# Kernel tuning notes

Hardware: AMD Instinct MI355X
Metric: run time of the kernel (lower is better)

The kernel has to match this reference:

```python
import jax, jax.numpy as jnp
import numpy as np

N = 500000
P = 50000
IN_DIM = 9
H = 128
EPS = 1e-5


def _xavier(key, fan_in, fan_out, gain=0.5):
    std = gain * np.sqrt(2.0 / (fan_in + fan_out))
    return jax.random.normal(key, (fan_in, fan_out), dtype=jnp.float32) * std


def setup_inputs() -> dict:
    key = jax.random.key(0)
    kx, kid, k0, k1, k2 = jax.random.split(key, 5)
    x = jax.random.normal(kx, (N, IN_DIM), dtype=jnp.float32)
    # guarantee every polyline id in [0, P) appears so torch.unique inverse == ids
    ids = jnp.concatenate([jnp.arange(P, dtype=jnp.int64),
                           jax.random.randint(kid, (N - P,), 0, P, dtype=jnp.int64)])
    polyline_ids = jax.random.permutation(kid, ids)
    inp = {"x": x, "polyline_ids": polyline_ids,
           "W0": _xavier(k0, IN_DIM, H), "b0": jnp.zeros((H,), jnp.float32),
           "g0": jnp.ones((H,), jnp.float32), "be0": jnp.zeros((H,), jnp.float32),
           "W1": _xavier(k1, 2 * H, H), "b1": jnp.zeros((H,), jnp.float32),
           "g1": jnp.ones((H,), jnp.float32), "be1": jnp.zeros((H,), jnp.float32),
           "W2": _xavier(k2, 2 * H, H), "b2": jnp.zeros((H,), jnp.float32),
           "g2": jnp.ones((H,), jnp.float32), "be2": jnp.zeros((H,), jnp.float32)}
    return inp


def _encoder(h, W, b, g, be):
    # Linear -> LayerNorm -> ReLU (Dropout is identity in eval)
    z = h @ W + b
    mu = jnp.mean(z, axis=-1, keepdims=True)
    var = jnp.var(z, axis=-1, keepdims=True)
    z = (z - mu) * jax.lax.rsqrt(var + EPS) * g + be
    return jax.nn.relu(z)


def _seg_max(h, ids):
    m = jax.ops.segment_max(h, ids, num_segments=P)
    # torch scatter_reduce(amax, include_self=False) leaves empty rows at 0
    return jnp.where(jnp.isfinite(m), m, 0.0)


def reference(x, polyline_ids, W0, b0, g0, be0, W1, b1, g1, be1, W2, b2, g2, be2):
    ids = polyline_ids.astype(jnp.int32)  # all of [0,P) present -> inverse == ids
    h = _encoder(x, W0, b0, g0, be0)  # [N, H]
    for (W, b, g, be) in ((W1, b1, g1, be1), (W2, b2, g2, be2)):
        agg = _seg_max(h, ids)[ids]               # [N, H] broadcast of per-polyline max
        h = _encoder(jnp.concatenate([h, agg], axis=-1), W, b, g, be)
    polyline_features = _seg_max(h, ids)          # [P, H]
    unique_polylines = jnp.arange(P, dtype=polyline_ids.dtype)
    return polyline_features, unique_polylines
```

## Files before the change

kernel.cpp:

```cpp
#include <hip/hip_runtime.h>
#include <hip/hip_bf16.h>
#include <hip/hip_fp16.h>

#define N_PTS 500000
#define P_POLY 50000
#define IN_DIM 9
#define HDIM 128
#define EPSV 1e-5f
#define NG 7813
#define CAPR 96
#define SLOTS 32
#define HS 136
#define XS 40

typedef __attribute__((ext_vector_type(8))) short short8;
typedef __attribute__((ext_vector_type(4))) float floatx4;

__device__ __forceinline__ unsigned short f2h(float f) {
  return __half_as_ushort(__float2half(f));
}
__device__ __forceinline__ float h2f(unsigned short u) {
  return __half2float(__ushort_as_half(u));
}
__device__ __forceinline__ unsigned int pkmax(unsigned int a, unsigned int b) {
  unsigned int r;
  asm("v_pk_max_f16 %0, %1, %2" : "=v"(r) : "v"(a), "v"(b));
  return r;
}

__global__ __launch_bounds__(256) void k_count(
    const int* __restrict__ ids, unsigned int* __restrict__ cnt)
{
  int i = blockIdx.x * blockDim.x + threadIdx.x;
  if (i < N_PTS) atomicAdd(&cnt[ids[i]], 1u);
}

__global__ __launch_bounds__(256) void k_scanwp(
    const unsigned int* __restrict__ cnt, unsigned int* __restrict__ btot,
    const float* __restrict__ W0, const float* __restrict__ W1,
    const float* __restrict__ W2,
    unsigned short* __restrict__ Wt0,
    unsigned short* __restrict__ Wt1, unsigned short* __restrict__ Wb1,
    unsigned short* __restrict__ Wt2, unsigned short* __restrict__ Wb2)
{
  if (blockIdx.x < 196) {
    __shared__ unsigned int s[256];
    int t = threadIdx.x;
    int i = blockIdx.x * 256 + t;
    s[t] = (i < P_POLY) ? cnt[i] : 0u;
    __syncthreads();
    for (int d = 128; d > 0; d >>= 1) {
      if (t < d) s[t] += s[t + d];
      __syncthreads();
    }
    if (t == 0) btot[blockIdx.x] = s[0];
  } else if (blockIdx.x < 324) {
    int bw = blockIdx.x - 196;
#pragma unroll
    for (int t = 0; t < 2; ++t) {
      int idx = (bw * 2 + t) * 256 + threadIdx.x;
      int sel = idx >> 14;
      int e = idx & 16383;
      int c = e & 127;
      int k = e >> 7;
      const float* W = (sel < 2) ? W1 : W2;
      unsigned short* O = sel == 0 ? Wt1 : sel == 1 ? Wb1 : sel == 2 ? Wt2 : Wb2;
      int kg = k + ((sel & 1) ? 128 : 0);
      O[c * 128 + k] = f2h(W[kg * 128 + c]);
    }
  } else {
#pragma unroll
    for (int t = 0; t < 16; ++t) {
      int idx = t * 256 + threadIdx.x;
      int c = idx & 127;
      int k = idx >> 7;
      Wt0[c * 32 + k] = (k < IN_DIM) ? f2h(W0[k * 128 + c]) : (unsigned short)0;
    }
  }
}

__global__ __launch_bounds__(256) void k_scan2(
    const unsigned int* __restrict__ cnt, const unsigned int* __restrict__ btot,
    unsigned int* __restrict__ offsets, unsigned int* __restrict__ woff)
{
  __shared__ unsigned int s[256];
  __shared__ unsigned int sbase;
  int b = blockIdx.x, t = threadIdx.x;
  int i = b * 256 + t;
  unsigned int v = (i < P_POLY) ? cnt[i] : 0u;
  s[t] = v;
  __syncthreads();
  for (int d = 1; d < 256; d <<= 1) {
    unsigned int tmp = (t >= d) ? s[t - d] : 0u;
    __syncthreads();
    s[t] += tmp;
    __syncthreads();
  }
  unsigned int incl = s[t];
  if (t == 0) {
    unsigned int base = 0;
    for (int j = 0; j < b; ++j) base += btot[j];
    sbase = base;
  }
  __syncthreads();
  unsigned int off = sbase + incl - v;
  if (i < P_POLY) {
    offsets[i] = off;
    woff[i] = off;
  }
}

__global__ __launch_bounds__(256) void k_place(
    const int* __restrict__ ids, unsigned int* __restrict__ woff,
    int* __restrict__ perm, int* __restrict__ pid_perm)
{
  int i = blockIdx.x * blockDim.x + threadIdx.x;
  if (i < N_PTS) {
    int id = ids[i];
    unsigned pos = atomicAdd(&woff[id], 1u);
    perm[pos] = i;
    pid_perm[pos] = id;
  }
}

__device__ __forceinline__ void ln_store(
    floatx4 (*acc)[2], int mtmax, unsigned short* sh, char* smisc,
    const float* __restrict__ bias, const float* __restrict__ gamma,
    const float* __restrict__ beta, int w, int l15, int l4)
{
  const int c0 = w * 32 + l15;
  const int c1 = c0 + 16;
  float bi0 = bias[c0], bi1 = bias[c1];
  float2* part = (float2*)smisc;
  float2* mufin = (float2*)(smisc + 3072);
#pragma unroll
  for (int mt = 0; mt < 6; ++mt) {
    if (mt < mtmax) {
      float s[4], ss[4];
#pragma unroll
      for (int r = 0; r < 4; ++r) {
        float z0 = acc[mt][0][r] + bi0;
        float z1 = acc[mt][1][r] + bi1;
        acc[mt][0][r] = z0;
        acc[mt][1][r] = z1;
        s[r] = z0 + z1;
        ss[r] = fmaf(z0, z0, z1 * z1);
      }
#pragma unroll
      for (int m = 1; m <= 8; m <<= 1) {
#pragma unroll
        for (int r = 0; r < 4; ++r) {
          s[r] += __shfl_xor(s[r], m);
          ss[r] += __shfl_xor(ss[r], m);
        }
      }
      if (l15 == 0) {
#pragma unroll
        for (int r = 0; r < 4; ++r)
          part[w * CAPR + mt * 16 + l4 * 4 + r] = make_float2(s[r], ss[r]);
      }
    }
  }
  __syncthreads();
  if (threadIdx.x < CAPR) {
    int rr = threadIdx.x;
    float2 qa = part[0 * CAPR + rr], qb = part[1 * CAPR + rr];
    float2 qc = part[2 * CAPR + rr], qd = part[3 * CAPR + rr];
    float S = qa.x + qb.x + qc.x + qd.x;
    float SS = qa.y + qb.y + qc.y + qd.y;
    float mu = S * (1.f / 128.f);
    float rv = rsqrtf(SS * (1.f / 128.f) - mu * mu + EPSV);
    mufin[rr] = make_float2(mu, rv);
  }
  __syncthreads();
  float ga0 = gamma[c0], ga1 = gamma[c1], bt0 = beta[c0], bt1 = beta[c1];
#pragma unroll
  for (int mt = 0; mt < 6; ++mt) {
    if (mt < mtmax) {
#pragma unroll
      for (int r = 0; r < 4; ++r) {
        int row = mt * 16 + l4 * 4 + r;
        float2 q = mufin[row];
        float v0 = fmaxf(fmaf((acc[mt][0][r] - q.x) * q.y, ga0, bt0), 0.f);
        float v1 = fmaxf(fmaf((acc[mt][1][r] - q.x) * q.y, ga1, bt1), 0.f);
        sh[row * HS + c0] = f2h(v0);
        sh[row * HS + c1] = f2h(v1);
      }
    }
  }
  __syncthreads();
}

__device__ __forceinline__ void enc_layer(
    unsigned short* sh, const unsigned short* sagg, const int* pid_loc, char* smisc,
    const unsigned short* __restrict__ Wt, const unsigned short* __restrict__ Wb,
    const float* __restrict__ bias, const float* __restrict__ gamma,
    const float* __restrict__ beta, int w, int l15, int l4, int koff, int nrows)
{
  const int c0 = w * 32 + l15;
  const int c1 = c0 + 16;
  const int mtmax = (nrows + 15) >> 4;
  floatx4 acc[6][2];
#pragma unroll
  for (int mt = 0; mt < 6; ++mt) {
    acc[mt][0] = (floatx4){0.f, 0.f, 0.f, 0.f};
    acc[mt][1] = (floatx4){0.f, 0.f, 0.f, 0.f};
  }
  int pl[6];
#pragma unroll
  for (int mt = 0; mt < 6; ++mt) pl[mt] = pid_loc[mt * 16 + l15];

#pragma unroll
  for (int kk = 0; kk < 4; ++kk) {
    short8 B0 = *reinterpret_cast<const short8*>(Wt + c0 * 128 + kk * 32 + koff);
    short8 B1 = *reinterpret_cast<const short8*>(Wt + c1 * 128 + kk * 32 + koff);
#pragma unroll
    for (int mt = 0; mt < 6; ++mt) {
      if (mt < mtmax) {
        short8 a = *reinterpret_cast<const short8*>(sh + (mt * 16 + l15) * HS + kk * 32 + koff);
        acc[mt][0] = __builtin_amdgcn_mfma_f32_16x16x32_f16(a, B0, acc[mt][0], 0, 0, 0);
        acc[mt][1] = __builtin_amdgcn_mfma_f32_16x16x32_f16(a, B1, acc[mt][1], 0, 0, 0);
      }
    }
  }
#pragma unroll
  for (int kk = 0; kk < 4; ++kk) {
    short8 B0 = *reinterpret_cast<const short8*>(Wb + c0 * 128 + kk * 32 + koff);
    short8 B1 = *reinterpret_cast<const short8*>(Wb + c1 * 128 + kk * 32 + koff);
#pragma unroll
    for (int mt = 0; mt < 6; ++mt) {
      if (mt < mtmax) {
        short8 a = *reinterpret_cast<const short8*>(sagg + pl[mt] * HS + kk * 32 + koff);
        acc[mt][0] = __builtin_amdgcn_mfma_f32_16x16x32_f16(a, B0, acc[mt][0], 0, 0, 0);
        acc[mt][1] = __builtin_amdgcn_mfma_f32_16x16x32_f16(a, B1, acc[mt][1], 0, 0, 0);
      }
    }
  }
  ln_store(acc, mtmax, sh, smisc, bias, gamma, beta, w, l15, l4);
}

__device__ __forceinline__ void enc_layer0(
    const unsigned short* xst, unsigned short* sh, char* smisc,
    const unsigned short* __restrict__ Wt0,
    const float* __restrict__ bias, const float* __restrict__ gamma,
    const float* __restrict__ beta, int w, int l15, int l4, int koff, int nrows)
{
  const int c0 = w * 32 + l15;
  const int c1 = c0 + 16;
  const int mtmax = (nrows + 15) >> 4;
  floatx4 acc[6][2];
#pragma unroll
  for (int mt = 0; mt < 6; ++mt) {
    acc[mt][0] = (floatx4){0.f, 0.f, 0.f, 0.f};
    acc[mt][1] = (floatx4){0.f, 0.f, 0.f, 0.f};
  }
  short8 B0 = *reinterpret_cast<const short8*>(Wt0 + c0 * 32 + koff);
  short8 B1 = *reinterpret_cast<const short8*>(Wt0 + c1 * 32 + koff);
#pragma unroll
  for (int mt = 0; mt < 6; ++mt) {
    if (mt < mtmax) {
      short8 a = *reinterpret_cast<const short8*>(xst + (mt * 16 + l15) * XS + koff);
      acc[mt][0] = __builtin_amdgcn_mfma_f32_16x16x32_f16(a, B0, acc[mt][0], 0, 0, 0);
      acc[mt][1] = __builtin_amdgcn_mfma_f32_16x16x32_f16(a, B1, acc[mt][1], 0, 0, 0);
    }
  }
  ln_store(acc, mtmax, sh, smisc, bias, gamma, beta, w, l15, l4);
}

__device__ __forceinline__ unsigned int slot_max(
    const unsigned short* sh, int ls, int n, int lane)
{
  const unsigned short* base = sh + ls * HS + 2 * lane;
  unsigned int m = 0u;
  for (int k = 0; k < n; k += 8) {
    unsigned int v[8];
#pragma unroll
    for (int j = 0; j < 8; ++j) {
      int kk = k + j;
      kk = kk < n - 1 ? kk : n - 1;
      v[j] = *reinterpret_cast<const unsigned int*>(base + kk * HS);
    }
    unsigned int a = pkmax(v[0], v[1]);
    unsigned int b = pkmax(v[2], v[3]);
    unsigned int c = pkmax(v[4], v[5]);
    unsigned int d = pkmax(v[6], v[7]);
    m = pkmax(m, pkmax(pkmax(a, b), pkmax(c, d)));
  }
  return m;
}

__global__ __launch_bounds__(256, 4) void k_fused(
    const float* __restrict__ x, const int* __restrict__ perm,
    const int* __restrict__ pid_perm, const unsigned int* __restrict__ offsets,
    const unsigned short* __restrict__ Wt0, const float* __restrict__ b0,
    const float* __restrict__ g0, const float* __restrict__ be0,
    const unsigned short* __restrict__ Wt1, const unsigned short* __restrict__ Wb1,
    const float* __restrict__ b1, const float* __restrict__ g1, const float* __restrict__ be1,
    const unsigned short* __restrict__ Wt2, const unsigned short* __restrict__ Wb2,
    const float* __restrict__ b2, const float* __restrict__ g2, const float* __restrict__ be2,
    float* __restrict__ out)
{
  __shared__ unsigned short sh[CAPR * HS];
  __shared__ unsigned short sagg[SLOTS * HS];
  __shared__ char smisc[3840];
  __shared__ short sl_off[SLOTS], sl_n[SLOTS];
  __shared__ int pid_loc[CAPR];

  const int g = blockIdx.x;
  const int j1 = g * 64;
  const int j2 = j1 + 64;

  int q = pid_perm[j1];
  int p_lo = q + ((int)offsets[q] < j1 ? 1 : 0);
  int p_hi, endrow;
  if (j2 >= N_PTS) {
    p_hi = P_POLY - 1;
    endrow = N_PTS;
  } else {
    int q2 = pid_perm[j2];
    p_hi = ((int)offsets[q2] < j2) ? q2 : q2 - 1;
    endrow = (p_hi + 1 < P_POLY) ? (int)offsets[p_hi + 1] : N_PTS;
  }
  int npoly = p_hi - p_lo + 1;
  if (npoly <= 0) return;
  if (npoly > SLOTS) npoly = SLOTS;
  const int rs = (int)offsets[p_lo];
  int nrows = endrow - rs;
  if (nrows > CAPR) nrows = CAPR;

  const int tid = threadIdx.x;
  const int lane = tid & 63;
  const int w = tid >> 6;
  const int l15 = lane & 15;
  const int l4 = lane >> 4;
  const int koff = l4 * 8;

  unsigned short* xst = sagg;
  for (int e = tid; e < nrows * 32; e += 256) {
    int r = e >> 5;
    int k = e & 31;
    float v = (k < IN_DIM) ? x[(size_t)perm[rs + r] * IN_DIM + k] : 0.f;
    xst[r * XS + k] = f2h(v);
  }
  for (int s = tid; s < npoly; s += 256) {
    int o = (int)offsets[p_lo + s];
    int e2 = (p_lo + s + 1 < P_POLY) ? (int)offsets[p_lo + s + 1] : N_PTS;
    int ls = o - rs;
    int n = e2 - o;
    if (n > CAPR - ls) n = CAPR - ls;
    sl_off[s] = (short)ls;
    sl_n[s] = (short)n;
  }
  for (int r = tid; r < CAPR; r += 256) {
    int v = 0;
    if (r < nrows) {
      v = pid_perm[rs + r] - p_lo;
      if (v >= SLOTS) v = SLOTS - 1;
      if (v < 0) v = 0;
    }
    pid_loc[r] = v;
  }
  __syncthreads();

  enc_layer0(xst, sh, smisc, Wt0, b0, g0, be0, w, l15, l4, koff, nrows);

  for (int s = w; s < npoly; s += 4) {
    unsigned int m = slot_max(sh, sl_off[s], sl_n[s], lane);
    *reinterpret_cast<unsigned int*>(sagg + s * HS + 2 * lane) = m;
  }
  __syncthreads();

  enc_layer(sh, sagg, pid_loc, smisc, Wt1, Wb1, b1, g1, be1, w, l15, l4, koff, nrows);

  for (int s = w; s < npoly; s += 4) {
    unsigned int m = slot_max(sh, sl_off[s], sl_n[s], lane);
    *reinterpret_cast<unsigned int*>(sagg + s * HS + 2 * lane) = m;
  }
  __syncthreads();

  enc_layer(sh, sagg, pid_loc, smisc, Wt2, Wb2, b2, g2, be2, w, l15, l4, koff, nrows);

  for (int s = w; s < npoly; s += 4) {
    unsigned int m = slot_max(sh, sl_off[s], sl_n[s], lane);
    float2 f = make_float2(h2f((unsigned short)(m & 0xFFFFu)),
                           h2f((unsigned short)(m >> 16)));
    int p = p_lo + s;
    *reinterpret_cast<float2*>(out + (size_t)p * 128 + 2 * lane) = f;
    if (lane == 0) out[(size_t)P_POLY * 128 + p] = (float)p;
  }
}

#define WS_CNT   0
#define WS_OFF   204800
#define WS_WOFF  409600
#define WS_BTOT  614400
#define WS_PERM  618496
#define WS_PID   2618496
#define WS_W     4618496
#define WS_NEED  4757760

__device__ __attribute__((aligned(256))) unsigned char g_fallback[WS_NEED];

extern "C" void kernel_launch(void* const* d_in, const int* in_sizes, int n_in,
                              void* d_out, int out_size, void* d_ws, size_t ws_size,
                              hipStream_t stream) {
  const float* x = (const float*)d_in[0];
  const int* ids = (const int*)d_in[1];
  const float* W0 = (const float*)d_in[2];
  const float* b0 = (const float*)d_in[3];
  const float* g0 = (const float*)d_in[4];
  const float* be0 = (const float*)d_in[5];
  const float* W1 = (const float*)d_in[6];
  const float* b1 = (const float*)d_in[7];
  const float* g1 = (const float*)d_in[8];
  const float* be1 = (const float*)d_in[9];
  const float* W2 = (const float*)d_in[10];
  const float* b2 = (const float*)d_in[11];
  const float* g2 = (const float*)d_in[12];
  const float* be2 = (const float*)d_in[13];

  char* ws = (char*)d_ws;
  if (ws_size < (size_t)WS_NEED) {
    void* p = nullptr;
    hipGetSymbolAddress(&p, HIP_SYMBOL(g_fallback));
    ws = (char*)p;
  }
  unsigned int* cnt = (unsigned int*)(ws + WS_CNT);
  unsigned int* offsets = (unsigned int*)(ws + WS_OFF);
  unsigned int* woff = (unsigned int*)(ws + WS_WOFF);
  unsigned int* btot = (unsigned int*)(ws + WS_BTOT);
  int* perm = (int*)(ws + WS_PERM);
  int* pid_perm = (int*)(ws + WS_PID);
  unsigned short* Wt1 = (unsigned short*)(ws + WS_W);
  unsigned short* Wb1 = (unsigned short*)(ws + WS_W + 32768);
  unsigned short* Wt2 = (unsigned short*)(ws + WS_W + 65536);
  unsigned short* Wb2 = (unsigned short*)(ws + WS_W + 98304);
  unsigned short* Wt0 = (unsigned short*)(ws + WS_W + 131072);
  float* out = (float*)d_out;

  hipMemsetAsync(cnt, 0, P_POLY * 4, stream);
  k_count<<<(N_PTS + 255) / 256, 256, 0, stream>>>(ids, cnt);
  k_scanwp<<<325, 256, 0, stream>>>(cnt, btot, W0, W1, W2, Wt0, Wt1, Wb1, Wt2, Wb2);
  k_scan2<<<196, 256, 0, stream>>>(cnt, btot, offsets, woff);
  k_place<<<(N_PTS + 255) / 256, 256, 0, stream>>>(ids, woff, perm, pid_perm);
  k_fused<<<NG, 256, 0, stream>>>(x, perm, pid_perm, offsets,
                                  Wt0, b0, g0, be0,
                                  Wt1, Wb1, b1, g1, be1,
                                  Wt2, Wb2, b2, g2, be2, out);
}
```

Measured before the change: 442.9 us.

## Merge preprocessing kernels into one cooperative kernel; inline LayerNorm stats

```diff
diff --git a/kernel.cpp b/kernel.cpp
--- a/kernel.cpp
+++ b/kernel.cpp
@@ -1,6 +1,9 @@
 #include <hip/hip_runtime.h>
 #include <hip/hip_bf16.h>
 #include <hip/hip_fp16.h>
+#include <hip/hip_cooperative_groups.h>
+
+namespace cg = cooperative_groups;
 
 #define N_PTS 500000
 #define P_POLY 50000
@@ -28,94 +31,83 @@
   return r;
 }
 
-__global__ __launch_bounds__(256) void k_count(
-    const int* __restrict__ ids, unsigned int* __restrict__ cnt)
-{
-  int i = blockIdx.x * blockDim.x + threadIdx.x;
-  if (i < N_PTS) atomicAdd(&cnt[ids[i]], 1u);
-}
-
-__global__ __launch_bounds__(256) void k_scanwp(
-    const unsigned int* __restrict__ cnt, unsigned int* __restrict__ btot,
+__global__ __launch_bounds__(256) void k_prep(
+    const int* __restrict__ ids,
+    unsigned int* __restrict__ cnt, unsigned int* __restrict__ btot,
+    unsigned int* __restrict__ offsets, unsigned int* __restrict__ woff,
+    int* __restrict__ perm, int* __restrict__ pid_perm,
     const float* __restrict__ W0, const float* __restrict__ W1,
     const float* __restrict__ W2,
     unsigned short* __restrict__ Wt0,
     unsigned short* __restrict__ Wt1, unsigned short* __restrict__ Wb1,
     unsigned short* __restrict__ Wt2, unsigned short* __restrict__ Wb2)
 {
+  cg::grid_group grid = cg::this_grid();
+  const int tid = threadIdx.x;
+  const int gid = blockIdx.x * 256 + tid;
+  const int gsz = gridDim.x * 256;
+
+  __shared__ unsigned int s[256];
+  __shared__ unsigned int sbase;
+
+  for (int i = gid; i < P_POLY; i += gsz) cnt[i] = 0u;
+  {
+    int idx = gid;
+    int sel = idx >> 14;
+    int e = idx & 16383;
+    int c = e & 127;
+    int k = e >> 7;
+    const float* W = (sel < 2) ? W1 : W2;
+    unsigned short* O = sel == 0 ? Wt1 : sel == 1 ? Wb1 : sel == 2 ? Wt2 : Wb2;
+    int kg = k + ((sel & 1) ? 128 : 0);
+    O[c * 128 + k] = f2h(W[kg * 128 + c]);
+  }
+  if (gid < 4096) {
+    int c = gid & 127, k = gid >> 7;
+    Wt0[c * 32 + k] = (k < IN_DIM) ? f2h(W0[k * 128 + c]) : (unsigned short)0;
+  }
+  grid.sync();
+
+  for (int i = gid; i < N_PTS; i += gsz) atomicAdd(&cnt[ids[i]], 1u);
+  grid.sync();
+
+  unsigned int v = 0, incl = 0;
   if (blockIdx.x < 196) {
-    __shared__ unsigned int s[256];
-    int t = threadIdx.x;
-    int i = blockIdx.x * 256 + t;
-    s[t] = (i < P_POLY) ? cnt[i] : 0u;
+    int i = blockIdx.x * 256 + tid;
+    v = (i < P_POLY) ? cnt[i] : 0u;
+    s[tid] = v;
+    __syncthreads();
+    for (int d = 1; d < 256; d <<= 1) {
+      unsigned int tmp = (tid >= d) ? s[tid - d] : 0u;
+      __syncthreads();
+      s[tid] += tmp;
+      __syncthreads();
+    }
+    incl = s[tid];
+    if (tid == 255) btot[blockIdx.x] = incl;
+  }
+  grid.sync();
+
+  if (blockIdx.x < 196) {
+    unsigned int bv = (tid < blockIdx.x) ? btot[tid] : 0u;
+    s[tid] = bv;
     __syncthreads();
     for (int d = 128; d > 0; d >>= 1) {
-      if (t < d) s[t] += s[t + d];
+      if (tid < d) s[tid] += s[tid + d];
       __syncthreads();
     }
-    if (t == 0) btot[blockIdx.x] = s[0];
-  } else if (blockIdx.x < 324) {
-    int bw = blockIdx.x - 196;
-#pragma unroll
-    for (int t = 0; t < 2; ++t) {
-      int idx = (bw * 2 + t) * 256 + threadIdx.x;
-      int sel = idx >> 14;
-      int e = idx & 16383;
-      int c = e & 127;
-      int k = e >> 7;
-      const float* W = (sel < 2) ? W1 : W2;
-      unsigned short* O = sel == 0 ? Wt1 : sel == 1 ? Wb1 : sel == 2 ? Wt2 : Wb2;
-      int kg = k + ((sel & 1) ? 128 : 0);
-      O[c * 128 + k] = f2h(W[kg * 128 + c]);
-    }
-  } else {
-#pragma unroll
-    for (int t = 0; t < 16; ++t) {
-      int idx = t * 256 + threadIdx.x;
-      int c = idx & 127;
-      int k = idx >> 7;
-      Wt0[c * 32 + k] = (k < IN_DIM) ? f2h(W0[k * 128 + c]) : (unsigned short)0;
-    }
-  }
-}
-
-__global__ __launch_bounds__(256) void k_scan2(
-    const unsigned int* __restrict__ cnt, const unsigned int* __restrict__ btot,
-    unsigned int* __restrict__ offsets, unsigned int* __restrict__ woff)
-{
-  __shared__ unsigned int s[256];
-  __shared__ unsigned int sbase;
-  int b = blockIdx.x, t = threadIdx.x;
-  int i = b * 256 + t;
-  unsigned int v = (i < P_POLY) ? cnt[i] : 0u;
-  s[t] = v;
-  __syncthreads();
-  for (int d = 1; d < 256; d <<= 1) {
-    unsigned int tmp = (t >= d) ? s[t - d] : 0u;
+    if (tid == 0) sbase = s[0];
     __syncthreads();
-    s[t] += tmp;
-    __syncthreads();
-  }
-  unsigned int incl = s[t];
-  if (t == 0) {
-    unsigned int base = 0;
-    for (int j = 0; j < b; ++j) base += btot[j];
-    sbase = base;
-  }
-  __syncthreads();
-  unsigned int off = sbase + incl - v;
-  if (i < P_POLY) {
-    offsets[i] = off;
-    woff[i] = off;
-  }
-}
-
-__global__ __launch_bounds__(256) void k_place(
-    const int* __restrict__ ids, unsigned int* __restrict__ woff,
-    int* __restrict__ perm, int* __restrict__ pid_perm)
-{
-  int i = blockIdx.x * blockDim.x + threadIdx.x;
-  if (i < N_PTS) {
+    unsigned int off = sbase + incl - v;
+    int i = blockIdx.x * 256 + tid;
+    if (i < P_POLY) {
+      offsets[i] = off;
+      woff[i] = off;
+    }
+  }
+  grid.sync();
+
+  for (int i = gid; i < N_PTS; i += gsz) {
     int id = ids[i];
     unsigned pos = atomicAdd(&woff[id], 1u);
     perm[pos] = i;
@@ -132,7 +124,6 @@
   const int c1 = c0 + 16;
   float bi0 = bias[c0], bi1 = bias[c1];
   float2* part = (float2*)smisc;
-  float2* mufin = (float2*)(smisc + 3072);
 #pragma unroll
   for (int mt = 0; mt < 6; ++mt) {
     if (mt < mtmax) {
@@ -162,17 +153,6 @@
     }
   }
   __syncthreads();
-  if (threadIdx.x < CAPR) {
-    int rr = threadIdx.x;
-    float2 qa = part[0 * CAPR + rr], qb = part[1 * CAPR + rr];
-    float2 qc = part[2 * CAPR + rr], qd = part[3 * CAPR + rr];
-    float S = qa.x + qb.x + qc.x + qd.x;
-    float SS = qa.y + qb.y + qc.y + qd.y;
-    float mu = S * (1.f / 128.f);
-    float rv = rsqrtf(SS * (1.f / 128.f) - mu * mu + EPSV);
-    mufin[rr] = make_float2(mu, rv);
-  }
-  __syncthreads();
   float ga0 = gamma[c0], ga1 = gamma[c1], bt0 = beta[c0], bt1 = beta[c1];
 #pragma unroll
   for (int mt = 0; mt < 6; ++mt) {
@@ -180,9 +160,14 @@
 #pragma unroll
       for (int r = 0; r < 4; ++r) {
         int row = mt * 16 + l4 * 4 + r;
-        float2 q = mufin[row];
-        float v0 = fmaxf(fmaf((acc[mt][0][r] - q.x) * q.y, ga0, bt0), 0.f);
-        float v1 = fmaxf(fmaf((acc[mt][1][r] - q.x) * q.y, ga1, bt1), 0.f);
+        float2 qa = part[0 * CAPR + row], qb = part[1 * CAPR + row];
+        float2 qc = part[2 * CAPR + row], qd = part[3 * CAPR + row];
+        float S = qa.x + qb.x + qc.x + qd.x;
+        float SS = qa.y + qb.y + qc.y + qd.y;
+        float mu = S * (1.f / 128.f);
+        float rv = rsqrtf(SS * (1.f / 128.f) - mu * mu + EPSV);
+        float v0 = fmaxf(fmaf((acc[mt][0][r] - mu) * rv, ga0, bt0), 0.f);
+        float v1 = fmaxf(fmaf((acc[mt][1][r] - mu) * rv, ga1, bt1), 0.f);
         sh[row * HS + c0] = f2h(v0);
         sh[row * HS + c1] = f2h(v1);
       }
@@ -302,7 +287,7 @@
 {
   __shared__ unsigned short sh[CAPR * HS];
   __shared__ unsigned short sagg[SLOTS * HS];
-  __shared__ char smisc[3840];
+  __shared__ char smisc[3072];
   __shared__ short sl_off[SLOTS], sl_n[SLOTS];
   __shared__ int pid_loc[CAPR];
 
@@ -404,8 +389,8 @@
 extern "C" void kernel_launch(void* const* d_in, const int* in_sizes, int n_in,
                               void* d_out, int out_size, void* d_ws, size_t ws_size,
                               hipStream_t stream) {
+  const int* ids = (const int*)d_in[1];
   const float* x = (const float*)d_in[0];
-  const int* ids = (const int*)d_in[1];
   const float* W0 = (const float*)d_in[2];
   const float* b0 = (const float*)d_in[3];
   const float* g0 = (const float*)d_in[4];
@@ -438,11 +423,12 @@
   unsigned short* Wt0 = (unsigned short*)(ws + WS_W + 131072);
   float* out = (float*)d_out;
 
-  hipMemsetAsync(cnt, 0, P_POLY * 4, stream);
-  k_count<<<(N_PTS + 255) / 256, 256, 0, stream>>>(ids, cnt);
-  k_scanwp<<<325, 256, 0, stream>>>(cnt, btot, W0, W1, W2, Wt0, Wt1, Wb1, Wt2, Wb2);
-  k_scan2<<<196, 256, 0, stream>>>(cnt, btot, offsets, woff);
-  k_place<<<(N_PTS + 255) / 256, 256, 0, stream>>>(ids, woff, perm, pid_perm);
+  void* args[] = {(void*)&ids, (void*)&cnt, (void*)&btot, (void*)&offsets,
+                  (void*)&woff, (void*)&perm, (void*)&pid_perm,
+                  (void*)&W0, (void*)&W1, (void*)&W2,
+                  (void*)&Wt0, (void*)&Wt1, (void*)&Wb1, (void*)&Wt2, (void*)&Wb2};
+  hipLaunchCooperativeKernel(reinterpret_cast<void*>(k_prep), dim3(256), dim3(256),
+                             args, 0, stream);
   k_fused<<<NG, 256, 0, stream>>>(x, perm, pid_perm, offsets,
                                   Wt0, b0, g0, be0,
                                   Wt1, Wb1, b1, g1, be1,
```

After: 595.5 us. 34.5% more time.
